# Kernel tuning notes

Hardware: AMD Instinct MI355X
Metric: run time of the kernel (lower is better)

Reference implementation:

```python
import jax, jax.numpy as jnp
import numpy as np
from jax import lax

IMG = 64
PAD = 2  # kernel_side=5, 'same' padding

def _conv(x, w, b):
    y = lax.conv_general_dilated(x, w, window_strides=(1, 1),
                                 padding=[(PAD, PAD), (PAD, PAD)],
                                 dimension_numbers=('NCHW', 'OIHW', 'NCHW'))
    return y + b[None, :, None, None]

def setup_inputs() -> dict:
    key = jax.random.key(0)
    ks = jax.random.split(key, 7)
    return {
        'x':  jax.random.normal(ks[0], (8, 1, IMG, IMG), dtype=jnp.float32),
        'w0': jax.random.normal(ks[1], (16, 1, 5, 5), dtype=jnp.float32) * 0.1,
        'b0': jax.random.normal(ks[2], (16,), dtype=jnp.float32) * 0.1,
        'w1': jax.random.normal(ks[3], (16, 16, 5, 5), dtype=jnp.float32) * 0.05,
        'b1': jax.random.normal(ks[4], (16,), dtype=jnp.float32) * 0.1,
        'w2': jax.random.normal(ks[5], (16, 16, 5, 5), dtype=jnp.float32) * 0.05,
        'b2': jax.random.normal(ks[6], (16,), dtype=jnp.float32) * 0.1,
        'kernel_mask': jnp.ones((IMG * IMG, IMG * IMG), dtype=jnp.float32),
    }

def reference(x, w0, b0, w1, b1, w2, b2, kernel_mask):
    # conv stack (no nonlinearity, as in the original module)
    for w, b in ((w0, b0), (w1, b1), (w2, b2)):
        x = _conv(x, w, b)
    B, C = x.shape[0], x.shape[1]
    means = x.mean(axis=1)                  # (B, H, W)
    stds = x.std(axis=1, ddof=1)            # torch.std is unbiased
    xc = (x - means[:, None]).reshape(B, C, -1)   # (B, C, N)
    s = stds.reshape(B, -1)                        # (B, N)
    # einsum('bci,bcj->bcij').mean(1) == channel-contracted matmul / C
    coupling = jnp.einsum('bci,bcj->bij', xc, xc) / C
    return coupling / (s[:, :, None] * s[:, None, :]) * kernel_mask
```

## Files before the change

### kernel.cpp

```cpp
#include <hip/hip_runtime.h>
#include <math.h>

#define IMG 64
#define NPX 4096
#define NC  16

typedef float v4f __attribute__((ext_vector_type(4)));

__global__ void repack_kernel(const float* __restrict__ w0,
                              const float* __restrict__ w1,
                              const float* __restrict__ w2,
                              float* __restrict__ wl0,
                              float* __restrict__ wl1,
                              float* __restrict__ wl2) {
    int idx = blockIdx.x * 256 + threadIdx.x;
    if (idx < 400) {
        int tap = idx >> 4, co = idx & 15;
        wl0[idx] = w0[co * 25 + tap];
    } else if (idx < 6800) {
        int e = idx - 400;
        int k = e >> 4, co = e & 15;
        wl1[e] = w1[co * 400 + k];
    } else if (idx < 13200) {
        int e = idx - 6800;
        int k = e >> 4, co = e & 15;
        wl2[e] = w2[co * 400 + k];
    }
}

__global__ void conv0_kernel(const float* __restrict__ x,
                             const float* __restrict__ wl0,
                             const float* __restrict__ b0,
                             float* __restrict__ y0) {
    __shared__ float tile[6 * 68];
    const int strip = blockIdx.x, b = blockIdx.y;
    const int r0 = strip * 2;
    const int tid = threadIdx.x;
    for (int f = tid; f < 6 * 68; f += 128) {
        int row = f / 68, col = f - row * 68;
        int gr = r0 - 2 + row, gc = col - 2;
        float v = 0.f;
        if (gr >= 0 && gr < IMG && gc >= 0 && gc < IMG)
            v = x[b * NPX + gr * IMG + gc];
        tile[f] = v;
    }
    __syncthreads();
    const int ri = tid >> 6, col = tid & 63;
    float acc[16];
#pragma unroll
    for (int co = 0; co < 16; ++co) acc[co] = b0[co];
#pragma unroll
    for (int kh = 0; kh < 5; ++kh) {
        float v[5];
#pragma unroll
        for (int kw = 0; kw < 5; ++kw) v[kw] = tile[(ri + kh) * 68 + col + kw];
#pragma unroll
        for (int kw = 0; kw < 5; ++kw) {
#pragma unroll
            for (int co = 0; co < 16; ++co)
                acc[co] = fmaf(wl0[(kh * 5 + kw) * 16 + co], v[kw], acc[co]);
        }
    }
    const int p = (r0 + ri) * IMG + col;
#pragma unroll
    for (int co = 0; co < 16; ++co)
        y0[(b * 16 + co) * NPX + p] = acc[co];
}

template <bool DO_STATS>
__global__ void conv16_kernel(const float* __restrict__ yin,
                              const float* __restrict__ wl,
                              const float* __restrict__ bias,
                              float* __restrict__ yout) {
    __shared__ float tile[16 * 6 * 68];
    const int strip = blockIdx.x, b = blockIdx.y;
    const int r0 = strip * 2;
    const int tid = threadIdx.x;
    for (int f = tid; f < 16 * 408; f += 128) {
        int ci = f / 408;
        int rem = f - ci * 408;
        int row = rem / 68, col = rem - row * 68;
        int gr = r0 - 2 + row, gc = col - 2;
        float v = 0.f;
        if (gr >= 0 && gr < IMG && gc >= 0 && gc < IMG)
            v = yin[(b * 16 + ci) * NPX + gr * IMG + gc];
        tile[f] = v;
    }
    __syncthreads();
    const int ri = tid >> 6, col = tid & 63;
    float acc[16];
#pragma unroll
    for (int co = 0; co < 16; ++co) acc[co] = bias[co];
    for (int ci = 0; ci < 16; ++ci) {
        const float* tci = &tile[ci * 408];
        const float* wci = &wl[ci * 25 * 16];
#pragma unroll
        for (int kh = 0; kh < 5; ++kh) {
            float v[5];
#pragma unroll
            for (int kw = 0; kw < 5; ++kw) v[kw] = tci[(ri + kh) * 68 + col + kw];
#pragma unroll
            for (int kw = 0; kw < 5; ++kw) {
#pragma unroll
                for (int co = 0; co < 16; ++co)
                    acc[co] = fmaf(wci[(kh * 5 + kw) * 16 + co], v[kw], acc[co]);
            }
        }
    }
    const int p = (r0 + ri) * IMG + col;
    if (DO_STATS) {
        float m = 0.f;
#pragma unroll
        for (int co = 0; co < 16; ++co) m += acc[co];
        m *= (1.f / 16.f);
        float var = 0.f;
#pragma unroll
        for (int co = 0; co < 16; ++co) {
            float d = acc[co] - m;
            var = fmaf(d, d, var);
        }
        var *= (1.f / 15.f);
        float inv = 0.25f / sqrtf(var);
#pragma unroll
        for (int co = 0; co < 16; ++co)
            yout[(b * 16 + co) * NPX + p] = (acc[co] - m) * inv;
    } else {
#pragma unroll
        for (int co = 0; co < 16; ++co)
            yout[(b * 16 + co) * NPX + p] = acc[co];
    }
}

__global__ void coupling_kernel(const float* __restrict__ z,
                                const float* __restrict__ mask,
                                float* __restrict__ out) {
    __shared__ float zis[8 * 16 * 16];
    const int tid = threadIdx.x;
    const int j0 = blockIdx.x * 1024 + tid * 4;
    const int i0 = blockIdx.y * 16;
    for (int f = tid; f < 2048; f += 256) {
        int c = f & 15, ii = (f >> 4) & 15, b = f >> 8;
        zis[f] = z[(b * 16 + c) * NPX + i0 + ii];
    }
    __syncthreads();
    for (int b = 0; b < 8; ++b) {
        v4f zj[16];
#pragma unroll
        for (int c = 0; c < 16; ++c)
            zj[c] = *(const v4f*)&z[(b * 16 + c) * NPX + j0];
#pragma unroll 4
        for (int ii = 0; ii < 16; ++ii) {
            const v4f mv = *(const v4f*)&mask[(size_t)(i0 + ii) * NPX + j0];
            const float* zr = &zis[(b * 16 + ii) * 16];
            v4f a = (v4f)(0.f);
#pragma unroll
            for (int c = 0; c < 16; ++c) {
                float s = zr[c];
                a.x = fmaf(s, zj[c].x, a.x);
                a.y = fmaf(s, zj[c].y, a.y);
                a.z = fmaf(s, zj[c].z, a.z);
                a.w = fmaf(s, zj[c].w, a.w);
            }
            a *= mv;
            __builtin_nontemporal_store(a,
                (v4f*)&out[((size_t)(b * NPX + i0 + ii)) * NPX + j0]);
        }
    }
}

extern "C" void kernel_launch(void* const* d_in, const int* in_sizes, int n_in,
                              void* d_out, int out_size, void* d_ws, size_t ws_size,
                              hipStream_t stream) {
    const float* x    = (const float*)d_in[0];
    const float* w0   = (const float*)d_in[1];
    const float* b0   = (const float*)d_in[2];
    const float* w1   = (const float*)d_in[3];
    const float* b1   = (const float*)d_in[4];
    const float* w2   = (const float*)d_in[5];
    const float* b2   = (const float*)d_in[6];
    const float* mask = (const float*)d_in[7];
    float* out = (float*)d_out;
    float* ws  = (float*)d_ws;

    float* wl0 = ws;
    float* wl1 = ws + 1024;
    float* wl2 = ws + 8192;
    float* y0  = ws + 16384;
    float* y1  = y0 + 524288;
    float* zz  = y1 + 524288;

    repack_kernel<<<52, 256, 0, stream>>>(w0, w1, w2, wl0, wl1, wl2);
    conv0_kernel<<<dim3(32, 8), 128, 0, stream>>>(x, wl0, b0, y0);
    conv16_kernel<false><<<dim3(32, 8), 128, 0, stream>>>(y0, wl1, b1, y1);
    conv16_kernel<true><<<dim3(32, 8), 128, 0, stream>>>(y1, wl2, b2, zz);
    coupling_kernel<<<dim3(4, 256), 256, 0, stream>>>(zz, mask, out);
}
```

Baseline: 735.1 us.

## Retile coupling kernel into 256x256 blocks with LDS-staged z_j and mask reuse

Restructures the coupling outer-product kernel into 256x256 output tiles per 512-thread block, staging all z_j columns for the tile in 128KB of LDS. Each thread loads eight mask rows once and reuses them across all eight batches. z_i values are read as wave-uniform scalars from global memory. The aim is to cut redundant mask and z reads and spread load overhead over a bounded output-write stream. The trade-off is heavy LDS use that limits occupancy to one block per CU, and only 256 blocks.

```diff
diff --git a/kernel.cpp b/kernel.cpp
--- a/kernel.cpp
+++ b/kernel.cpp
@@ -131,39 +131,52 @@
     }
 }
 
-__global__ void coupling_kernel(const float* __restrict__ z,
-                                const float* __restrict__ mask,
-                                float* __restrict__ out) {
-    __shared__ float zis[8 * 16 * 16];
+__global__ __launch_bounds__(512) void coupling_kernel(
+        const float* __restrict__ z,
+        const float* __restrict__ mask,
+        float* __restrict__ out) {
+    __shared__ float zj_lds[8 * 16 * 256];
     const int tid = threadIdx.x;
-    const int j0 = blockIdx.x * 1024 + tid * 4;
-    const int i0 = blockIdx.y * 16;
-    for (int f = tid; f < 2048; f += 256) {
-        int c = f & 15, ii = (f >> 4) & 15, b = f >> 8;
-        zis[f] = z[(b * 16 + c) * NPX + i0 + ii];
+    const int j0 = blockIdx.x * 256;
+    const int i0 = blockIdx.y * 256;
+
+    for (int f = tid; f < 8 * 16 * 64; f += 512) {
+        int jq = f & 63;
+        int bc = f >> 6;
+        v4f v = *(const v4f*)&z[(size_t)bc * NPX + j0 + jq * 4];
+        *(v4f*)&zj_lds[bc * 256 + jq * 4] = v;
     }
     __syncthreads();
-    for (int b = 0; b < 8; ++b) {
-        v4f zj[16];
-#pragma unroll
-        for (int c = 0; c < 16; ++c)
-            zj[c] = *(const v4f*)&z[(b * 16 + c) * NPX + j0];
-#pragma unroll 4
-        for (int ii = 0; ii < 16; ++ii) {
-            const v4f mv = *(const v4f*)&mask[(size_t)(i0 + ii) * NPX + j0];
-            const float* zr = &zis[(b * 16 + ii) * 16];
-            v4f a = (v4f)(0.f);
+
+    const int jq4 = (tid & 63) * 4;
+    const int ir = __builtin_amdgcn_readfirstlane(tid >> 6);
+#pragma unroll 1
+    for (int g = 0; g < 4; ++g) {
+        const int iiB = ir * 32 + g * 8;
+        v4f mv[8];
+#pragma unroll
+        for (int k = 0; k < 8; ++k)
+            mv[k] = *(const v4f*)&mask[(size_t)(i0 + iiB + k) * NPX + j0 + jq4];
+#pragma unroll 1
+        for (int b = 0; b < 8; ++b) {
+            const float* zi = z + (size_t)(b * 16) * NPX + i0 + iiB;
+            v4f acc[8];
+#pragma unroll
+            for (int k = 0; k < 8; ++k) acc[k] = (v4f)(0.f);
 #pragma unroll
             for (int c = 0; c < 16; ++c) {
-                float s = zr[c];
-                a.x = fmaf(s, zj[c].x, a.x);
-                a.y = fmaf(s, zj[c].y, a.y);
-                a.z = fmaf(s, zj[c].z, a.z);
-                a.w = fmaf(s, zj[c].w, a.w);
+                v4f zjv = *(const v4f*)&zj_lds[(b * 16 + c) * 256 + jq4];
+                const float* zr = zi + c * NPX;
+#pragma unroll
+                for (int k = 0; k < 8; ++k)
+                    acc[k] += zjv * zr[k];
             }
-            a *= mv;
-            __builtin_nontemporal_store(a,
-                (v4f*)&out[((size_t)(b * NPX + i0 + ii)) * NPX + j0]);
+#pragma unroll
+            for (int k = 0; k < 8; ++k) {
+                v4f r = acc[k] * mv[k];
+                __builtin_nontemporal_store(r,
+                    (v4f*)&out[(size_t)(b * NPX + i0 + iiB + k) * NPX + j0 + jq4]);
+            }
         }
     }
 }
@@ -193,5 +206,5 @@
     conv0_kernel<<<dim3(32, 8), 128, 0, stream>>>(x, wl0, b0, y0);
     conv16_kernel<false><<<dim3(32, 8), 128, 0, stream>>>(y0, wl1, b1, y1);
     conv16_kernel<true><<<dim3(32, 8), 128, 0, stream>>>(y1, wl2, b2, zz);
-    coupling_kernel<<<dim3(4, 256), 256, 0, stream>>>(zz, mask, out);
-}
+    coupling_kernel<<<dim3(16, 16), 512, 0, stream>>>(zz, mask, out);
+}
```

Result: faster. 677.8 us (-7.8%).
